# Kernel tuning notes

Measured on AMD Instinct MI355X. Metric: run time of the kernel, lower is better.

## Reference

```python
import jax, jax.numpy as jnp
import numpy as np

EPS = 1e-12  # torch F.normalize eps

def _l2n(x, axis):
    n = jnp.linalg.norm(x, axis=axis, keepdims=True)
    return x / jnp.maximum(n, EPS)

def setup_inputs() -> dict:
    key = jax.random.key(0)
    ks = jax.random.split(key, 11)
    B, N, D = 8, 4096, 512
    s = 1.0 / np.sqrt(D)
    return {
        'a': jax.random.normal(ks[0], (B, N, D), jnp.float32),
        'b': jax.random.normal(ks[1], (B, N, D), jnp.float32),
        'Wq': jax.random.normal(ks[2], (D, D), jnp.float32) * s,
        'bq': jax.random.normal(ks[3], (D,), jnp.float32) * s,
        'Wk': jax.random.normal(ks[4], (D, D), jnp.float32) * s,
        'bk': jax.random.normal(ks[5], (D,), jnp.float32) * s,
        'w_g': jax.random.normal(ks[6], (D, 1), jnp.float32),
        'Wp': jax.random.normal(ks[7], (D, D), jnp.float32) * s,
        'bp': jax.random.normal(ks[8], (D,), jnp.float32) * s,
        'Wf': jax.random.normal(ks[9], (D, D), jnp.float32) * s,
        'bf': jax.random.normal(ks[10], (D,), jnp.float32) * s,
    }

def reference(a, b, Wq, bq, Wk, bk, w_g, Wp, bp, Wf, bf):
    D = a.shape[-1]
    scale = D ** (-0.5)
    query = _l2n(jnp.einsum('bnd,ed->bne', a, Wq) + bq, axis=-1)   # [B,N,D]
    key = _l2n(jnp.einsum('bnd,ed->bne', b, Wk) + bk, axis=-1)     # [B,N,D]
    A = (query @ w_g) * scale                                      # [B,N,1]
    A = _l2n(A, axis=1)                                            # normalize over seq
    G = jnp.sum(A * query, axis=1)                                 # [B,D] learned pooling
    gk = G[:, None, :] * key                                       # broadcast [B,N,D]
    out = jnp.einsum('bnd,ed->bne', gk, Wp) + bp + query           # residual
    out = jnp.einsum('bnd,ed->bne', out, Wf) + bf
    return out
```

## Files before the change

kernel.cpp:

```cpp
#include <hip/hip_runtime.h>
#include <stdint.h>

#define DD 512
#define MTOT 32768

typedef float f32x4 __attribute__((ext_vector_type(4)));
typedef __bf16 bf16x8 __attribute__((ext_vector_type(8)));

static __device__ __forceinline__ unsigned short f2bf(float f) {
  union { float f; unsigned int u; } c; c.f = f;
  unsigned int r = c.u + 0x7fffu + ((c.u >> 16) & 1u);
  return (unsigned short)(r >> 16);
}
static __device__ __forceinline__ float bf2f(unsigned short h) {
  union { unsigned int u; float f; } c; c.u = ((unsigned int)h) << 16;
  return c.f;
}

union FragU { uint4 u; bf16x8 b; };

static __device__ __forceinline__ void load_lds16(const void* g, void* l) {
  __builtin_amdgcn_global_load_lds(
      (const __attribute__((address_space(1))) void*)g,
      (__attribute__((address_space(3))) void*)l, 16, 0, 0);
}

__global__ __launch_bounds__(256) void cvtab_k(const float* __restrict__ a,
    const float* __restrict__ b, unsigned short* __restrict__ da,
    unsigned short* __restrict__ db) {
  const float* s = blockIdx.y ? b : a;
  unsigned short* d = blockIdx.y ? db : da;
  size_t i = ((size_t)blockIdx.x * 256 + threadIdx.x) * 8;
  f32x4 f0 = *(const f32x4*)(s + i);
  f32x4 f1 = *(const f32x4*)(s + i + 4);
  union { uint4 u; unsigned short h[8]; } pk;
  pk.h[0] = f2bf(f0.x); pk.h[1] = f2bf(f0.y);
  pk.h[2] = f2bf(f0.z); pk.h[3] = f2bf(f0.w);
  pk.h[4] = f2bf(f1.x); pk.h[5] = f2bf(f1.y);
  pk.h[6] = f2bf(f1.z); pk.h[7] = f2bf(f1.w);
  *(uint4*)(d + i) = pk.u;
}

__global__ __launch_bounds__(256) void cvt3w_k(const float* __restrict__ W0,
    const float* __restrict__ W1, const float* __restrict__ W2,
    unsigned short* __restrict__ D0, unsigned short* __restrict__ D1,
    unsigned short* __restrict__ D2, float* __restrict__ stats) {
  int slab = blockIdx.x >> 8;
  if (slab == 3) {
    int i = ((blockIdx.x - 768) * 256 + threadIdx.x) * 4;
    *(float4*)(stats + i) = make_float4(0.f, 0.f, 0.f, 0.f);
    return;
  }
  int off = ((blockIdx.x & 255) * 256 + threadIdx.x) * 4;
  const float* s = slab == 0 ? W0 : slab == 1 ? W1 : W2;
  unsigned short* d = slab == 0 ? D0 : slab == 1 ? D1 : D2;
  float4 f = *(const float4*)(s + off);
  ushort4 h;
  h.x = f2bf(f.x); h.y = f2bf(f.y); h.z = f2bf(f.z); h.w = f2bf(f.w);
  *(ushort4*)(d + off) = h;
}

__global__ __launch_bounds__(256) void scalew_k(const float* __restrict__ Wp,
    const float* __restrict__ G, unsigned short* __restrict__ out) {
  int i = (blockIdx.x * 256 + threadIdx.x) * 4;
  int b = i >> 18;
  int rem = i & 262143;
  int d = rem & 511;
  float4 w = *(const float4*)(Wp + rem);
  float4 g = *(const float4*)(G + b * DD + d);
  ushort4 h;
  h.x = f2bf(w.x * g.x); h.y = f2bf(w.y * g.y);
  h.z = f2bf(w.z * g.z); h.w = f2bf(w.w * g.w);
  *(ushort4*)(out + i) = h;
}

template<int BBATCH, int EMODE>
__global__ __launch_bounds__(256) void gemm_k(
    const unsigned short* __restrict__ X,
    const unsigned short* __restrict__ Wb,
    const float* __restrict__ bias,
    const unsigned short* __restrict__ Qadd,
    const float* __restrict__ wg,
    float* __restrict__ ssq,
    float* __restrict__ Pdot,
    const float* __restrict__ qinv,
    const float* __restrict__ kinv,
    void* __restrict__ Cv) {
  __shared__ unsigned short As[128 * 64];
  __shared__ unsigned short Bs[128 * 64];
  const int tid = threadIdx.x;
  const int lane = tid & 63, wave = tid >> 6;
  const int row0 = blockIdx.x * 128, col0 = blockIdx.y * 128;
  const unsigned short* W = Wb + (BBATCH ? (size_t)(row0 >> 12) * 262144 : 0);

  const int sr = lane >> 3;
  const int scol = ((lane & 7) ^ sr) * 8;
  const unsigned short* Ag = X + (size_t)(row0 + wave * 32 + sr) * DD + scol;
  const unsigned short* Bg = W + (size_t)(col0 + wave * 32 + sr) * DD + scol;
  const int ldsb = wave * 32 * 64;

  const int fr = lane & 15, quad = lane >> 4;
  const int wr = (wave >> 1) * 64, wc = (wave & 1) * 64;
  const int sw0 = ((quad ^ (fr & 7)) * 8);
  const int sw1 = (((quad + 4) ^ (fr & 7)) * 8);

  f32x4 acc[4][4] = {};

  for (int k0 = 0; k0 < DD; k0 += 64) {
#pragma unroll
    for (int q = 0; q < 4; q++) {
      load_lds16(Ag + (size_t)q * 8 * DD + k0, As + ldsb + q * 8 * 64);
      load_lds16(Bg + (size_t)q * 8 * DD + k0, Bs + ldsb + q * 8 * 64);
    }
    __syncthreads();
#pragma unroll
    for (int kk = 0; kk < 2; kk++) {
      const int sw = kk ? sw1 : sw0;
      bf16x8 af[4], bfr[4];
#pragma unroll
      for (int i = 0; i < 4; i++) {
        FragU u; u.u = *(const uint4*)&As[(wr + i * 16 + fr) * 64 + sw];
        af[i] = u.b;
      }
#pragma unroll
      for (int j = 0; j < 4; j++) {
        FragU u; u.u = *(const uint4*)&Bs[(wc + j * 16 + fr) * 64 + sw];
        bfr[j] = u.b;
      }
#pragma unroll
      for (int i = 0; i < 4; i++)
#pragma unroll
        for (int j = 0; j < 4; j++)
          acc[i][j] = __builtin_amdgcn_mfma_f32_16x16x32_bf16(af[i], bfr[j], acc[i][j], 0, 0, 0);
    }
    __syncthreads();
  }

  const int colbase = col0 + wc + fr;
  float bv4[4];
#pragma unroll
  for (int j = 0; j < 4; j++) bv4[j] = bias[colbase + j * 16];
  float wg4[4];
  if (EMODE == 1) {
#pragma unroll
    for (int j = 0; j < 4; j++) wg4[j] = wg[colbase + j * 16];
  }
#pragma unroll
  for (int i = 0; i < 4; i++) {
#pragma unroll
    for (int r = 0; r < 4; r++) {
      const int row = row0 + wr + i * 16 + quad * 4 + r;
      float ki = 1.f, qi = 1.f;
      if (EMODE == 3) { ki = kinv[row]; qi = qinv[row]; }
      float ssum = 0.f, dsum = 0.f;
#pragma unroll
      for (int j = 0; j < 4; j++) {
        size_t idx = (size_t)row * DD + colbase + j * 16;
        float v;
        if (EMODE == 3) v = acc[i][j][r] * ki + bv4[j] + qi * bf2f(Qadd[idx]);
        else            v = acc[i][j][r] + bv4[j];
        if (EMODE != 4) ((unsigned short*)Cv)[idx] = f2bf(v);
        else            ((float*)Cv)[idx] = v;
        if (EMODE == 1 || EMODE == 2) ssum += v * v;
        if (EMODE == 1) dsum += v * wg4[j];
      }
      if (EMODE == 1 || EMODE == 2) {
#pragma unroll
        for (int m = 1; m < 16; m <<= 1) ssum += __shfl_xor(ssum, m, 64);
        if (EMODE == 1) {
#pragma unroll
          for (int m = 1; m < 16; m <<= 1) dsum += __shfl_xor(dsum, m, 64);
        }
        if (fr == 0) {
          atomicAdd(&ssq[row], ssum);
          if (EMODE == 1) atomicAdd(&Pdot[row], dsum);
        }
      }
    }
  }
}

__global__ __launch_bounds__(512) void finstat_k(const float* __restrict__ ssqQ,
    const float* __restrict__ ssqK, const float* __restrict__ P,
    float* __restrict__ qinv, float* __restrict__ kinv,
    float* __restrict__ Araw2, float* __restrict__ sinv, float* __restrict__ G) {
  const int b = blockIdx.x, t = threadIdx.x;
  G[b * DD + t] = 0.f;
  float ss = 0.f;
  for (int i = t; i < 4096; i += 512) {
    int n = b * 4096 + i;
    float qi = 1.0f / fmaxf(sqrtf(ssqQ[n]), 1e-12f);
    float ki = 1.0f / fmaxf(sqrtf(ssqK[n]), 1e-12f);
    qinv[n] = qi; kinv[n] = ki;
    float A = P[n] * qi;
    Araw2[n] = A * qi;
    ss += A * A;
  }
#pragma unroll
  for (int m = 1; m < 64; m <<= 1) ss += __shfl_xor(ss, m, 64);
  __shared__ float sred[8];
  if ((t & 63) == 0) sred[t >> 6] = ss;
  __syncthreads();
  if (t == 0) {
    float tot = 0.f;
    for (int i = 0; i < 8; i++) tot += sred[i];
    sinv[b] = 1.0f / fmaxf(sqrtf(tot), 1e-12f);
  }
}

__global__ __launch_bounds__(256) void pool_k(const float* __restrict__ Araw2,
    const float* __restrict__ sinv, const unsigned short* __restrict__ Q,
    float* __restrict__ G) {
  const int b = blockIdx.x >> 5;
  const int chunk = blockIdx.x & 31;
  const int rbase = b * 4096 + chunk * 128;
  const float si = sinv[b];
  const int t = threadIdx.x;
  float a0 = 0.f, a1 = 0.f;
  for (int r = 0; r < 128; r++) {
    float w = Araw2[rbase + r] * si;
    const unsigned short* qr = Q + (size_t)(rbase + r) * DD;
    a0 += w * bf2f(qr[t]);
    a1 += w * bf2f(qr[t + 256]);
  }
  atomicAdd(&G[b * DD + t], a0);
  atomicAdd(&G[b * DD + t + 256], a1);
}

extern "C" void kernel_launch(void* const* d_in, const int* in_sizes, int n_in,
                              void* d_out, int out_size, void* d_ws, size_t ws_size,
                              hipStream_t stream) {
  const float* a   = (const float*)d_in[0];
  const float* b   = (const float*)d_in[1];
  const float* Wq  = (const float*)d_in[2];
  const float* bq  = (const float*)d_in[3];
  const float* Wk  = (const float*)d_in[4];
  const float* bk  = (const float*)d_in[5];
  const float* wg  = (const float*)d_in[6];
  const float* Wp  = (const float*)d_in[7];
  const float* bp  = (const float*)d_in[8];
  const float* Wf  = (const float*)d_in[9];
  const float* bfb = (const float*)d_in[10];

  const size_t WELEM = 262144;
  const size_t MD = (size_t)MTOT * DD;

  unsigned short* B0 = (unsigned short*)d_ws;
  unsigned short* B1 = B0 + MD;
  unsigned short* B2 = B1 + MD;
  unsigned short* Wqb = B2 + MD;
  unsigned short* Wkb = Wqb + WELEM;
  unsigned short* Wfb = Wkb + WELEM;
  unsigned short* Wps = Wfb + WELEM;
  float* stats = (float*)(Wps + 8 * WELEM);
  float* ssqQ  = stats;
  float* ssqK  = stats + MTOT;
  float* Pd    = stats + 2 * MTOT;
  float* qinv  = stats + 3 * MTOT;
  float* kinv  = stats + 4 * MTOT;
  float* Araw2 = stats + 5 * MTOT;
  float* sinv  = stats + 6 * MTOT;
  float* G     = sinv + 64;

  cvtab_k<<<dim3(8192, 2), dim3(256), 0, stream>>>(a, b, B0, B1);
  cvt3w_k<<<dim3(864), dim3(256), 0, stream>>>(Wq, Wk, Wf, Wqb, Wkb, Wfb, stats);
  gemm_k<0, 1><<<dim3(256, 4), dim3(256), 0, stream>>>(
      B0, Wqb, bq, nullptr, wg, ssqQ, Pd, nullptr, nullptr, B2);
  gemm_k<0, 2><<<dim3(256, 4), dim3(256), 0, stream>>>(
      B1, Wkb, bk, nullptr, nullptr, ssqK, nullptr, nullptr, nullptr, B0);
  finstat_k<<<dim3(8), dim3(512), 0, stream>>>(ssqQ, ssqK, Pd, qinv, kinv, Araw2, sinv, G);
  pool_k<<<dim3(256), dim3(256), 0, stream>>>(Araw2, sinv, B2, G);
  scalew_k<<<dim3(2048), dim3(256), 0, stream>>>(Wp, G, Wps);
  gemm_k<1, 3><<<dim3(256, 4), dim3(256), 0, stream>>>(
      B0, Wps, bp, B2, nullptr, nullptr, nullptr, qinv, kinv, B1);
  gemm_k<0, 4><<<dim3(256, 4), dim3(256), 0, stream>>>(
      B1, Wfb, bfb, nullptr, nullptr, nullptr, nullptr, nullptr, nullptr, d_out);
}
```

Before: 320.8 us.

## Fuse conversion kernels, batch Q/K GEMMs, and merge stats with pooling

The input and weight fp32-to-bf16 conversions and the stats zeroing now run in one kernel, with each thread in the input part converting eight strided chunks. The Q and K projection GEMMs share one launch with twice the grid, so the two independent GEMMs fill the GPU together. The 8-block serial finstat kernel is folded into the pooling kernel: every pool block recomputes the per-batch sequence-norm reduction on its own and writes its slice of qinv/kinv, which removes the Araw2/sinv buffers and a launch. The cost is redundant reduction work in each pooling block and an extra bf16 activation buffer.

Result: no change. 325.8 us (+1.5%).

```diff
diff --git a/kernel.cpp b/kernel.cpp
--- a/kernel.cpp
+++ b/kernel.cpp
@@ -25,39 +25,44 @@
       (__attribute__((address_space(3))) void*)l, 16, 0, 0);
 }
 
-__global__ __launch_bounds__(256) void cvtab_k(const float* __restrict__ a,
-    const float* __restrict__ b, unsigned short* __restrict__ da,
-    unsigned short* __restrict__ db) {
-  const float* s = blockIdx.y ? b : a;
-  unsigned short* d = blockIdx.y ? db : da;
-  size_t i = ((size_t)blockIdx.x * 256 + threadIdx.x) * 8;
-  f32x4 f0 = *(const f32x4*)(s + i);
-  f32x4 f1 = *(const f32x4*)(s + i + 4);
-  union { uint4 u; unsigned short h[8]; } pk;
-  pk.h[0] = f2bf(f0.x); pk.h[1] = f2bf(f0.y);
-  pk.h[2] = f2bf(f0.z); pk.h[3] = f2bf(f0.w);
-  pk.h[4] = f2bf(f1.x); pk.h[5] = f2bf(f1.y);
-  pk.h[6] = f2bf(f1.z); pk.h[7] = f2bf(f1.w);
-  *(uint4*)(d + i) = pk.u;
-}
-
-__global__ __launch_bounds__(256) void cvt3w_k(const float* __restrict__ W0,
-    const float* __restrict__ W1, const float* __restrict__ W2,
+__global__ __launch_bounds__(256) void cvt_all_k(
+    const float* __restrict__ a, const float* __restrict__ b,
+    const float* __restrict__ W0, const float* __restrict__ W1,
+    const float* __restrict__ W2,
+    unsigned short* __restrict__ da, unsigned short* __restrict__ db,
     unsigned short* __restrict__ D0, unsigned short* __restrict__ D1,
     unsigned short* __restrict__ D2, float* __restrict__ stats) {
-  int slab = blockIdx.x >> 8;
-  if (slab == 3) {
-    int i = ((blockIdx.x - 768) * 256 + threadIdx.x) * 4;
+  const int gx = blockIdx.x, tid = threadIdx.x;
+  if (gx < 768) {
+    int slab = gx >> 8;
+    int off = ((gx & 255) * 256 + tid) * 4;
+    const float* s = slab == 0 ? W0 : slab == 1 ? W1 : W2;
+    unsigned short* d = slab == 0 ? D0 : slab == 1 ? D1 : D2;
+    float4 f = *(const float4*)(s + off);
+    ushort4 h;
+    h.x = f2bf(f.x); h.y = f2bf(f.y); h.z = f2bf(f.z); h.w = f2bf(f.w);
+    *(ushort4*)(d + off) = h;
+  } else if (gx < 868) {
+    int i = ((gx - 768) * 256 + tid) * 4;
     *(float4*)(stats + i) = make_float4(0.f, 0.f, 0.f, 0.f);
-    return;
-  }
-  int off = ((blockIdx.x & 255) * 256 + threadIdx.x) * 4;
-  const float* s = slab == 0 ? W0 : slab == 1 ? W1 : W2;
-  unsigned short* d = slab == 0 ? D0 : slab == 1 ? D1 : D2;
-  float4 f = *(const float4*)(s + off);
-  ushort4 h;
-  h.x = f2bf(f.x); h.y = f2bf(f.y); h.z = f2bf(f.z); h.w = f2bf(f.w);
-  *(ushort4*)(d + off) = h;
+  } else {
+    const int u = gx - 868;
+    const float* s = (u >> 10) ? b : a;
+    unsigned short* d = (u >> 10) ? db : da;
+    const size_t base = ((size_t)(u & 1023) * 256 + tid) * 8;
+#pragma unroll
+    for (int t = 0; t < 8; t++) {
+      size_t i = base + (size_t)t * 2097152;
+      f32x4 f0 = *(const f32x4*)(s + i);
+      f32x4 f1 = *(const f32x4*)(s + i + 4);
+      union { uint4 u4; unsigned short h[8]; } pk;
+      pk.h[0] = f2bf(f0.x); pk.h[1] = f2bf(f0.y);
+      pk.h[2] = f2bf(f0.z); pk.h[3] = f2bf(f0.w);
+      pk.h[4] = f2bf(f1.x); pk.h[5] = f2bf(f1.y);
+      pk.h[6] = f2bf(f1.z); pk.h[7] = f2bf(f1.w);
+      *(uint4*)(d + i) = pk.u4;
+    }
+  }
 }
 
 __global__ __launch_bounds__(256) void scalew_k(const float* __restrict__ Wp,
@@ -74,77 +79,136 @@
   *(ushort4*)(out + i) = h;
 }
 
+static __device__ __forceinline__ void gemm_core(
+    const unsigned short* __restrict__ X, const unsigned short* __restrict__ W,
+    int row0, int col0, unsigned short* As, unsigned short* Bs,
+    f32x4 (&acc)[4][4]) {
+  const int tid = threadIdx.x;
+  const int lane = tid & 63, wave = tid >> 6;
+  const int sr = lane >> 3;
+  const int scol = ((lane & 7) ^ sr) * 8;
+  const unsigned short* Ag = X + (size_t)(row0 + wave * 32 + sr) * DD + scol;
+  const unsigned short* Bg = W + (size_t)(col0 + wave * 32 + sr) * DD + scol;
+  const int ldsb = wave * 32 * 64;
+  const int fr = lane & 15, quad = lane >> 4;
+  const int wr = (wave >> 1) * 64, wc = (wave & 1) * 64;
+  const int sw0 = ((quad ^ (fr & 7)) * 8);
+  const int sw1 = (((quad + 4) ^ (fr & 7)) * 8);
+
+  for (int k0 = 0; k0 < DD; k0 += 64) {
+#pragma unroll
+    for (int q = 0; q < 4; q++) {
+      load_lds16(Ag + (size_t)q * 8 * DD + k0, As + ldsb + q * 8 * 64);
+      load_lds16(Bg + (size_t)q * 8 * DD + k0, Bs + ldsb + q * 8 * 64);
+    }
+    __syncthreads();
+#pragma unroll
+    for (int kk = 0; kk < 2; kk++) {
+      const int sw = kk ? sw1 : sw0;
+      bf16x8 af[4], bfr[4];
+#pragma unroll
+      for (int i = 0; i < 4; i++) {
+        FragU u; u.u = *(const uint4*)&As[(wr + i * 16 + fr) * 64 + sw];
+        af[i] = u.b;
+      }
+#pragma unroll
+      for (int j = 0; j < 4; j++) {
+        FragU u; u.u = *(const uint4*)&Bs[(wc + j * 16 + fr) * 64 + sw];
+        bfr[j] = u.b;
+      }
+#pragma unroll
+      for (int i = 0; i < 4; i++)
+#pragma unroll
+        for (int j = 0; j < 4; j++)
+          acc[i][j] = __builtin_amdgcn_mfma_f32_16x16x32_bf16(af[i], bfr[j], acc[i][j], 0, 0, 0);
+    }
+    __syncthreads();
+  }
+}
+
+__global__ __launch_bounds__(256) void gemm_qk_k(
+    const unsigned short* __restrict__ Xq, const unsigned short* __restrict__ Xk,
+    const unsigned short* __restrict__ Wqw, const unsigned short* __restrict__ Wkw,
+    const float* __restrict__ bq, const float* __restrict__ bk,
+    const float* __restrict__ wg,
+    float* __restrict__ ssqQ, float* __restrict__ ssqK, float* __restrict__ Pdot,
+    unsigned short* __restrict__ Cq, unsigned short* __restrict__ Ck) {
+  __shared__ unsigned short As[128 * 64];
+  __shared__ unsigned short Bs[128 * 64];
+  const int isK = blockIdx.x >> 8;
+  const int row0 = (blockIdx.x & 255) * 128, col0 = blockIdx.y * 128;
+  const unsigned short* X = isK ? Xk : Xq;
+  const unsigned short* W = isK ? Wkw : Wqw;
+  const float* bias = isK ? bk : bq;
+  float* ssq = isK ? ssqK : ssqQ;
+  unsigned short* C = isK ? Ck : Cq;
+
+  f32x4 acc[4][4] = {};
+  gemm_core(X, W, row0, col0, As, Bs, acc);
+
+  const int lane = threadIdx.x & 63, wave = threadIdx.x >> 6;
+  const int fr = lane & 15, quad = lane >> 4;
+  const int wr = (wave >> 1) * 64, wc = (wave & 1) * 64;
+  const int colbase = col0 + wc + fr;
+  float bv4[4], wg4[4];
+#pragma unroll
+  for (int j = 0; j < 4; j++) bv4[j] = bias[colbase + j * 16];
+  if (!isK) {
+#pragma unroll
+    for (int j = 0; j < 4; j++) wg4[j] = wg[colbase + j * 16];
+  }
+#pragma unroll
+  for (int i = 0; i < 4; i++) {
+#pragma unroll
+    for (int r = 0; r < 4; r++) {
+      const int row = row0 + wr + i * 16 + quad * 4 + r;
+      float ssum = 0.f, dsum = 0.f;
+#pragma unroll
+      for (int j = 0; j < 4; j++) {
+        size_t idx = (size_t)row * DD + colbase + j * 16;
+        float v = acc[i][j][r] + bv4[j];
+        C[idx] = f2bf(v);
+        ssum += v * v;
+        if (!isK) dsum += v * wg4[j];
+      }
+#pragma unroll
+      for (int m = 1; m < 16; m <<= 1) ssum += __shfl_xor(ssum, m, 64);
+      if (!isK) {
+#pragma unroll
+        for (int m = 1; m < 16; m <<= 1) dsum += __shfl_xor(dsum, m, 64);
+      }
+      if (fr == 0) {
+        atomicAdd(&ssq[row], ssum);
+        if (!isK) atomicAdd(&Pdot[row], dsum);
+      }
+    }
+  }
+}
+
 template<int BBATCH, int EMODE>
 __global__ __launch_bounds__(256) void gemm_k(
     const unsigned short* __restrict__ X,
     const unsigned short* __restrict__ Wb,
     const float* __restrict__ bias,
     const unsigned short* __restrict__ Qadd,
-    const float* __restrict__ wg,
-    float* __restrict__ ssq,
-    float* __restrict__ Pdot,
     const float* __restrict__ qinv,
     const float* __restrict__ kinv,
     void* __restrict__ Cv) {
   __shared__ unsigned short As[128 * 64];
   __shared__ unsigned short Bs[128 * 64];
-  const int tid = threadIdx.x;
-  const int lane = tid & 63, wave = tid >> 6;
   const int row0 = blockIdx.x * 128, col0 = blockIdx.y * 128;
   const unsigned short* W = Wb + (BBATCH ? (size_t)(row0 >> 12) * 262144 : 0);
 
-  const int sr = lane >> 3;
-  const int scol = ((lane & 7) ^ sr) * 8;
-  const unsigned short* Ag = X + (size_t)(row0 + wave * 32 + sr) * DD + scol;
-  const unsigned short* Bg = W + (size_t)(col0 + wave * 32 + sr) * DD + scol;
-  const int ldsb = wave * 32 * 64;
-
+  f32x4 acc[4][4] = {};
+  gemm_core(X, W, row0, col0, As, Bs, acc);
+
+  const int lane = threadIdx.x & 63, wave = threadIdx.x >> 6;
   const int fr = lane & 15, quad = lane >> 4;
   const int wr = (wave >> 1) * 64, wc = (wave & 1) * 64;
-  const int sw0 = ((quad ^ (fr & 7)) * 8);
-  const int sw1 = (((quad + 4) ^ (fr & 7)) * 8);
-
-  f32x4 acc[4][4] = {};
-
-  for (int k0 = 0; k0 < DD; k0 += 64) {
-#pragma unroll
-    for (int q = 0; q < 4; q++) {
-      load_lds16(Ag + (size_t)q * 8 * DD + k0, As + ldsb + q * 8 * 64);
-      load_lds16(Bg + (size_t)q * 8 * DD + k0, Bs + ldsb + q * 8 * 64);
-    }
-    __syncthreads();
-#pragma unroll
-    for (int kk = 0; kk < 2; kk++) {
-      const int sw = kk ? sw1 : sw0;
-      bf16x8 af[4], bfr[4];
-#pragma unroll
-      for (int i = 0; i < 4; i++) {
-        FragU u; u.u = *(const uint4*)&As[(wr + i * 16 + fr) * 64 + sw];
-        af[i] = u.b;
-      }
-#pragma unroll
-      for (int j = 0; j < 4; j++) {
-        FragU u; u.u = *(const uint4*)&Bs[(wc + j * 16 + fr) * 64 + sw];
-        bfr[j] = u.b;
-      }
-#pragma unroll
-      for (int i = 0; i < 4; i++)
-#pragma unroll
-        for (int j = 0; j < 4; j++)
-          acc[i][j] = __builtin_amdgcn_mfma_f32_16x16x32_bf16(af[i], bfr[j], acc[i][j], 0, 0, 0);
-    }
-    __syncthreads();
-  }
-
   const int colbase = col0 + wc + fr;
   float bv4[4];
 #pragma unroll
   for (int j = 0; j < 4; j++) bv4[j] = bias[colbase + j * 16];
-  float wg4[4];
-  if (EMODE == 1) {
-#pragma unroll
-    for (int j = 0; j < 4; j++) wg4[j] = wg[colbase + j * 16];
-  }
 #pragma unroll
   for (int i = 0; i < 4; i++) {
 #pragma unroll
@@ -152,79 +216,67 @@
       const int row = row0 + wr + i * 16 + quad * 4 + r;
       float ki = 1.f, qi = 1.f;
       if (EMODE == 3) { ki = kinv[row]; qi = qinv[row]; }
-      float ssum = 0.f, dsum = 0.f;
 #pragma unroll
       for (int j = 0; j < 4; j++) {
         size_t idx = (size_t)row * DD + colbase + j * 16;
-        float v;
-        if (EMODE == 3) v = acc[i][j][r] * ki + bv4[j] + qi * bf2f(Qadd[idx]);
-        else            v = acc[i][j][r] + bv4[j];
-        if (EMODE != 4) ((unsigned short*)Cv)[idx] = f2bf(v);
-        else            ((float*)Cv)[idx] = v;
-        if (EMODE == 1 || EMODE == 2) ssum += v * v;
-        if (EMODE == 1) dsum += v * wg4[j];
-      }
-      if (EMODE == 1 || EMODE == 2) {
-#pragma unroll
-        for (int m = 1; m < 16; m <<= 1) ssum += __shfl_xor(ssum, m, 64);
-        if (EMODE == 1) {
-#pragma unroll
-          for (int m = 1; m < 16; m <<= 1) dsum += __shfl_xor(dsum, m, 64);
+        if (EMODE == 3) {
+          float v = acc[i][j][r] * ki + bv4[j] + qi * bf2f(Qadd[idx]);
+          ((unsigned short*)Cv)[idx] = f2bf(v);
+        } else {
+          ((float*)Cv)[idx] = acc[i][j][r] + bv4[j];
         }
-        if (fr == 0) {
-          atomicAdd(&ssq[row], ssum);
-          if (EMODE == 1) atomicAdd(&Pdot[row], dsum);
-        }
-      }
-    }
-  }
-}
-
-__global__ __launch_bounds__(512) void finstat_k(const float* __restrict__ ssqQ,
-    const float* __restrict__ ssqK, const float* __restrict__ P,
-    float* __restrict__ qinv, float* __restrict__ kinv,
-    float* __restrict__ Araw2, float* __restrict__ sinv, float* __restrict__ G) {
-  const int b = blockIdx.x, t = threadIdx.x;
-  G[b * DD + t] = 0.f;
+      }
+    }
+  }
+}
+
+__global__ __launch_bounds__(256) void pool2_k(
+    const float* __restrict__ ssqQ, const float* __restrict__ ssqK,
+    const float* __restrict__ P, float* __restrict__ qinv,
+    float* __restrict__ kinv, const unsigned short* __restrict__ Q,
+    float* __restrict__ G) {
+  const int b = blockIdx.x >> 5, chunk = blockIdx.x & 31;
+  const int t = threadIdx.x, lane = t & 63, wave = t >> 6;
+  __shared__ float sred[4];
+  __shared__ float gred[4][512];
+
   float ss = 0.f;
-  for (int i = t; i < 4096; i += 512) {
+  for (int i = t; i < 4096; i += 256) {
     int n = b * 4096 + i;
     float qi = 1.0f / fmaxf(sqrtf(ssqQ[n]), 1e-12f);
-    float ki = 1.0f / fmaxf(sqrtf(ssqK[n]), 1e-12f);
-    qinv[n] = qi; kinv[n] = ki;
     float A = P[n] * qi;
-    Araw2[n] = A * qi;
     ss += A * A;
   }
 #pragma unroll
   for (int m = 1; m < 64; m <<= 1) ss += __shfl_xor(ss, m, 64);
-  __shared__ float sred[8];
-  if ((t & 63) == 0) sred[t >> 6] = ss;
+  if (lane == 0) sred[wave] = ss;
+  if (t < 128) {
+    int n = b * 4096 + chunk * 128 + t;
+    qinv[n] = 1.0f / fmaxf(sqrtf(ssqQ[n]), 1e-12f);
+    kinv[n] = 1.0f / fmaxf(sqrtf(ssqK[n]), 1e-12f);
+  }
   __syncthreads();
-  if (t == 0) {
-    float tot = 0.f;
-    for (int i = 0; i < 8; i++) tot += sred[i];
-    sinv[b] = 1.0f / fmaxf(sqrtf(tot), 1e-12f);
-  }
-}
-
-__global__ __launch_bounds__(256) void pool_k(const float* __restrict__ Araw2,
-    const float* __restrict__ sinv, const unsigned short* __restrict__ Q,
-    float* __restrict__ G) {
-  const int b = blockIdx.x >> 5;
-  const int chunk = blockIdx.x & 31;
-  const int rbase = b * 4096 + chunk * 128;
-  const float si = sinv[b];
-  const int t = threadIdx.x;
-  float a0 = 0.f, a1 = 0.f;
-  for (int r = 0; r < 128; r++) {
-    float w = Araw2[rbase + r] * si;
-    const unsigned short* qr = Q + (size_t)(rbase + r) * DD;
-    a0 += w * bf2f(qr[t]);
-    a1 += w * bf2f(qr[t + 256]);
-  }
-  atomicAdd(&G[b * DD + t], a0);
-  atomicAdd(&G[b * DD + t + 256], a1);
+  const float sinv_b =
+      1.0f / fmaxf(sqrtf(sred[0] + sred[1] + sred[2] + sred[3]), 1e-12f);
+
+  float acc[8] = {};
+  const int r0 = b * 4096 + chunk * 128 + wave * 32;
+  for (int r = 0; r < 32; r++) {
+    const int n = r0 + r;
+    float qi = 1.0f / fmaxf(sqrtf(ssqQ[n]), 1e-12f);
+    float wrow = P[n] * qi * qi * sinv_b;
+    uint4 u = *(const uint4*)(Q + (size_t)n * DD + lane * 8);
+    const unsigned short* h = (const unsigned short*)&u;
+#pragma unroll
+    for (int j = 0; j < 8; j++) acc[j] += wrow * bf2f(h[j]);
+  }
+#pragma unroll
+  for (int j = 0; j < 8; j++) gred[wave][lane * 8 + j] = acc[j];
+  __syncthreads();
+  float g0 = gred[0][t] + gred[1][t] + gred[2][t] + gred[3][t];
+  float g1 = gred[0][t + 256] + gred[1][t + 256] + gred[2][t + 256] + gred[3][t + 256];
+  atomicAdd(&G[b * DD + t], g0);
+  atomicAdd(&G[b * DD + t + 256], g1);
 }
 
 extern "C" void kernel_launch(void* const* d_in, const int* in_sizes, int n_in,
@@ -248,7 +300,8 @@
   unsigned short* B0 = (unsigned short*)d_ws;
   unsigned short* B1 = B0 + MD;
   unsigned short* B2 = B1 + MD;
-  unsigned short* Wqb = B2 + MD;
+  unsigned short* B3 = B2 + MD;
+  unsigned short* Wqb = B3 + MD;
   unsigned short* Wkb = Wqb + WELEM;
   unsigned short* Wfb = Wkb + WELEM;
   unsigned short* Wps = Wfb + WELEM;
@@ -256,23 +309,18 @@
   float* ssqQ  = stats;
   float* ssqK  = stats + MTOT;
   float* Pd    = stats + 2 * MTOT;
-  float* qinv  = stats + 3 * MTOT;
-  float* kinv  = stats + 4 * MTOT;
-  float* Araw2 = stats + 5 * MTOT;
-  float* sinv  = stats + 6 * MTOT;
-  float* G     = sinv + 64;
-
-  cvtab_k<<<dim3(8192, 2), dim3(256), 0, stream>>>(a, b, B0, B1);
-  cvt3w_k<<<dim3(864), dim3(256), 0, stream>>>(Wq, Wk, Wf, Wqb, Wkb, Wfb, stats);
-  gemm_k<0, 1><<<dim3(256, 4), dim3(256), 0, stream>>>(
-      B0, Wqb, bq, nullptr, wg, ssqQ, Pd, nullptr, nullptr, B2);
-  gemm_k<0, 2><<<dim3(256, 4), dim3(256), 0, stream>>>(
-      B1, Wkb, bk, nullptr, nullptr, ssqK, nullptr, nullptr, nullptr, B0);
-  finstat_k<<<dim3(8), dim3(512), 0, stream>>>(ssqQ, ssqK, Pd, qinv, kinv, Araw2, sinv, G);
-  pool_k<<<dim3(256), dim3(256), 0, stream>>>(Araw2, sinv, B2, G);
+  float* G     = stats + 3 * MTOT;
+  float* qinv  = G + 4096;
+  float* kinv  = qinv + MTOT;
+
+  cvt_all_k<<<dim3(2916), dim3(256), 0, stream>>>(
+      a, b, Wq, Wk, Wf, B0, B1, Wqb, Wkb, Wfb, stats);
+  gemm_qk_k<<<dim3(512, 4), dim3(256), 0, stream>>>(
+      B0, B1, Wqb, Wkb, bq, bk, wg, ssqQ, ssqK, Pd, B2, B3);
+  pool2_k<<<dim3(256), dim3(256), 0, stream>>>(ssqQ, ssqK, Pd, qinv, kinv, B2, G);
   scalew_k<<<dim3(2048), dim3(256), 0, stream>>>(Wp, G, Wps);
   gemm_k<1, 3><<<dim3(256, 4), dim3(256), 0, stream>>>(
-      B0, Wps, bp, B2, nullptr, nullptr, nullptr, qinv, kinv, B1);
+      B3, Wps, bp, B2, qinv, kinv, B0);
   gemm_k<0, 4><<<dim3(256, 4), dim3(256), 0, stream>>>(
-      B1, Wfb, bfb, nullptr, nullptr, nullptr, nullptr, nullptr, nullptr, d_out);
-}
+      B0, Wfb, bfb, nullptr, nullptr, nullptr, d_out);
+}
```
